# Kernel tuning notes

Measured on AMD Instinct MI355X. Metric: run time of the kernel, lower is better.

Reference implementation:

```python
import jax, jax.numpy as jnp
import numpy as np

D_MODEL = 1024
NUM_HEADS = 16


def setup_inputs() -> dict:
    key = jax.random.key(0)
    ks = jax.random.split(key, 5)
    B, S, D = 4, 2048, D_MODEL
    scale = 0.02  # realistic init scale so logits stay well-conditioned
    return {
        "x": jax.random.normal(ks[0], (B, S, D), dtype=jnp.float32),
        "Wq": jax.random.normal(ks[1], (D, D), dtype=jnp.float32) * scale,
        "Wk": jax.random.normal(ks[2], (D, D), dtype=jnp.float32) * scale,
        "Wv": jax.random.normal(ks[3], (D, D), dtype=jnp.float32) * scale,
        "Wo": jax.random.normal(ks[4], (D, D), dtype=jnp.float32) * scale,
    }


def reference(x, Wq, Wk, Wv, Wo):
    # x: (B, S, D). Weights are (d_out, d_in) as in the torch module.
    B, S, D = x.shape
    H = NUM_HEADS
    dk = D // H

    # Projections: einsum('oi,bli->blo') == x @ W.T
    q = jnp.einsum("oi,bsi->bso", Wq, x).reshape(B, S, H, dk).transpose(0, 2, 1, 3)
    k = jnp.einsum("oi,bsi->bso", Wk, x).reshape(B, S, H, dk).transpose(0, 2, 1, 3)
    v = jnp.einsum("oi,bsi->bso", Wv, x).reshape(B, S, H, dk).transpose(0, 2, 1, 3)

    # Scaled dot-product scores per head: (B, H, S, S)
    scores = jnp.einsum("bhqd,bhkd->bhqk", q, k) / jnp.sqrt(jnp.asarray(dk, x.dtype))

    # Causal mask (True = keep); masked entries get -inf (matches inf-subtraction)
    causal = jnp.tril(jnp.ones((S, S), dtype=bool))
    scores = jnp.where(causal, scores, -jnp.inf)

    attn = jax.nn.softmax(scores, axis=-1)

    out = jnp.einsum("bhqk,bhkd->bhqd", attn, v)  # (B, H, S, dk)
    out = out.transpose(0, 2, 1, 3).reshape(B, S, D)  # concat heads

    # Output projection: einsum('oi,bli->blo')
    return jnp.einsum("oi,bsi->bso", Wo, out)
```

## Files before the change

### kernel.cpp

```cpp
#include <hip/hip_runtime.h>
#include <hip/hip_bf16.h>

typedef unsigned short u16;
typedef __attribute__((ext_vector_type(8))) short short8;
typedef __attribute__((ext_vector_type(4))) float f32x4;

#if __has_builtin(__builtin_amdgcn_exp2f)
#define EXP2F(x) __builtin_amdgcn_exp2f(x)
#else
#define EXP2F(x) exp2f(x)
#endif

__device__ __forceinline__ float bf2f(u16 v) {
    union { unsigned u; float f; } c; c.u = ((unsigned)v) << 16; return c.f;
}
__device__ __forceinline__ u16 f2bf(float f) {
    union { float f; unsigned u; } c; c.f = f;
    unsigned r = c.u + 0x7fffu + ((c.u >> 16) & 1u);
    return (u16)(r >> 16);
}
__device__ __forceinline__ uint4 pack8(const float4 a, const float4 b) {
    uint4 r;
    r.x = (unsigned)f2bf(a.x) | ((unsigned)f2bf(a.y) << 16);
    r.y = (unsigned)f2bf(a.z) | ((unsigned)f2bf(a.w) << 16);
    r.z = (unsigned)f2bf(b.x) | ((unsigned)f2bf(b.y) << 16);
    r.w = (unsigned)f2bf(b.z) | ((unsigned)f2bf(b.w) << 16);
    return r;
}
__device__ __forceinline__ void gl_lds16(const u16* g, u16* l) {
    __builtin_amdgcn_global_load_lds((const __attribute__((address_space(1))) unsigned int*)g,
                                     (__attribute__((address_space(3))) unsigned int*)l, 16, 0, 0);
}

__global__ __launch_bounds__(256) void convert_all(const float* __restrict__ x,
                                                   const float* __restrict__ wq,
                                                   const float* __restrict__ wk,
                                                   const float* __restrict__ wv,
                                                   const float* __restrict__ wo,
                                                   u16* xb, u16* wqb, u16* wkb, u16* wvb, u16* wob) {
    size_t i8 = ((size_t)blockIdx.x * 256 + threadIdx.x) * 8;
    const float* src; u16* dst; size_t off;
    if (i8 < 8388608) { src = x; dst = xb; off = i8; }
    else {
        size_t idx = i8 - 8388608;
        int w = (int)(idx >> 20); off = idx & 1048575;
        src = (w == 0) ? wq : (w == 1) ? wk : (w == 2) ? wv : wo;
        dst = (w == 0) ? wqb : (w == 1) ? wkb : (w == 2) ? wvb : wob;
    }
    float4 a = *(const float4*)&src[off];
    float4 b = *(const float4*)&src[off + 4];
    *(uint4*)&dst[off] = pack8(a, b);
}

__device__ __forceinline__ void gemm_core(const u16* __restrict__ A, const u16* __restrict__ B,
                                          int m0, int n0, u16* As, u16* Bs, f32x4 acc[4][4]) {
    const int tid = threadIdx.x;
    const int wv = tid >> 6, lane = tid & 63, lr = lane & 15, quad = lane >> 4;
    const int srow = lane >> 3;
    const int scg  = (lane & 7) ^ srow;
    const int wm = (wv >> 1) * 64, wn = (wv & 1) * 64;

    for (int kt = 0; kt < 1024; kt += 64) {
        __syncthreads();
        #pragma unroll
        for (int t = 0; t < 4; ++t) {
            int r = wv * 32 + t * 8;
            gl_lds16(&A[(size_t)(m0 + r + srow) * 1024 + kt + scg * 8], &As[r * 64]);
            gl_lds16(&B[(size_t)(n0 + r + srow) * 1024 + kt + scg * 8], &Bs[r * 64]);
        }
        __syncthreads();
        #pragma unroll
        for (int c = 0; c < 2; ++c) {
            short8 af[4], bf[4];
            #pragma unroll
            for (int mi = 0; mi < 4; ++mi)
                af[mi] = *(const short8*)&As[(wm + mi * 16 + lr) * 64 + (((c * 4 + quad) ^ (lr & 7)) * 8)];
            #pragma unroll
            for (int ni = 0; ni < 4; ++ni)
                bf[ni] = *(const short8*)&Bs[(wn + ni * 16 + lr) * 64 + (((c * 4 + quad) ^ (lr & 7)) * 8)];
            #pragma unroll
            for (int mi = 0; mi < 4; ++mi)
                #pragma unroll
                for (int ni = 0; ni < 4; ++ni)
                    acc[mi][ni] = __builtin_amdgcn_mfma_f32_16x16x32_bf16(af[mi], bf[ni], acc[mi][ni], 0, 0, 0);
        }
    }
}

__device__ __forceinline__ void core_dual(const u16* __restrict__ A,
                                          const u16* __restrict__ B0,
                                          const u16* __restrict__ B1,
                                          int m0, int n0a, int n0b,
                                          u16* As, u16* Bs0, u16* Bs1,
                                          f32x4 acc0[2][4], f32x4 acc1[2][4]) {
    const int tid = threadIdx.x;
    const int wid = tid >> 6, lane = tid & 63, lr = lane & 15, quad = lane >> 4;
    const int srow = lane >> 3;
    const int scg  = (lane & 7) ^ srow;
    const int wm = (wid >> 1) * 32, wn = (wid & 1) * 64;
    const int r0 = wid * 16;

    for (int kt = 0; kt < 1024; kt += 64) {
        __syncthreads();
        #pragma unroll
        for (int h = 0; h < 2; ++h) {
            int r = r0 + h * 8;
            gl_lds16(&A [(size_t)(m0  + r + srow) * 1024 + kt + scg * 8], &As [r * 64]);
            gl_lds16(&B0[(size_t)(n0a + r + srow) * 1024 + kt + scg * 8], &Bs0[r * 64]);
            gl_lds16(&B1[(size_t)(n0b + r + srow) * 1024 + kt + scg * 8], &Bs1[r * 64]);
        }
        __syncthreads();
        #pragma unroll
        for (int c = 0; c < 2; ++c) {
            short8 af[2], bf[4];
            #pragma unroll
            for (int mi = 0; mi < 2; ++mi)
                af[mi] = *(const short8*)&As[(wm + mi * 16 + lr) * 64 + (((c * 4 + quad) ^ (lr & 7)) * 8)];
            #pragma unroll
            for (int ni = 0; ni < 4; ++ni)
                bf[ni] = *(const short8*)&Bs0[(wn + ni * 16 + lr) * 64 + (((c * 4 + quad) ^ (lr & 7)) * 8)];
            #pragma unroll
            for (int mi = 0; mi < 2; ++mi)
                #pragma unroll
                for (int ni = 0; ni < 4; ++ni)
                    acc0[mi][ni] = __builtin_amdgcn_mfma_f32_16x16x32_bf16(af[mi], bf[ni], acc0[mi][ni], 0, 0, 0);
            #pragma unroll
            for (int ni = 0; ni < 4; ++ni)
                bf[ni] = *(const short8*)&Bs1[(wn + ni * 16 + lr) * 64 + (((c * 4 + quad) ^ (lr & 7)) * 8)];
            #pragma unroll
            for (int mi = 0; mi < 2; ++mi)
                #pragma unroll
                for (int ni = 0; ni < 4; ++ni)
                    acc1[mi][ni] = __builtin_amdgcn_mfma_f32_16x16x32_bf16(af[mi], bf[ni], acc1[mi][ni], 0, 0, 0);
        }
    }
}

__global__ __launch_bounds__(512, 4) void gemm_qkv(const u16* __restrict__ xb,
                                                   const u16* __restrict__ wq,
                                                   const u16* __restrict__ wk,
                                                   const u16* __restrict__ wv,
                                                   u16* __restrict__ Qb, u16* __restrict__ Kb,
                                                   u16* __restrict__ Vtb) {
    __shared__ __align__(16) u16 As [8192];
    __shared__ __align__(16) u16 Bs0[8192];
    __shared__ __align__(16) u16 Bs1[8192];
    const int bid = blockIdx.x;

    f32x4 acc0[2][4], acc1[2][4];
    #pragma unroll
    for (int a = 0; a < 2; ++a)
        #pragma unroll
        for (int b = 0; b < 4; ++b) { acc0[a][b] = 0; acc1[a][b] = 0; }

    const int lane = threadIdx.x & 63, lr = lane & 15, quad = lane >> 4;
    const int wid = threadIdx.x >> 6;
    const int wm = (wid >> 1) * 32, wn = (wid & 1) * 64;

    if (bid < 512) {
        const int xcd = bid & 7;
        const int i   = bid >> 3;
        const int m0  = (xcd * 8 + (i & 7)) * 128;
        const int n0  = (i >> 3) * 128;
        core_dual(xb, wq, wk, m0, n0, n0, As, Bs0, Bs1, acc0, acc1);
        #pragma unroll
        for (int mi = 0; mi < 2; ++mi)
            #pragma unroll
            for (int ni = 0; ni < 4; ++ni)
                #pragma unroll
                for (int reg = 0; reg < 4; ++reg) {
                    int row = m0 + wm + mi * 16 + quad * 4 + reg;
                    int col = n0 + wn + ni * 16 + lr;
                    int bhh = (row >> 11) * 16 + (col >> 6);
                    size_t o = (size_t)bhh * 131072 + (size_t)(row & 2047) * 64 + (col & 63);
                    Qb[o] = f2bf(acc0[mi][ni][reg] * 0.18033688f);
                    Kb[o] = f2bf(acc1[mi][ni][reg]);
                }
    } else {
        const int t   = bid - 512;
        const int xcd = t & 7;
        const int j   = t >> 3;
        const int m0  = (j & 7) * 128;
        const int np  = xcd * 4 + (j >> 3);
        const int n0a = np * 256, n0b = np * 256 + 128;
        core_dual(wv, xb, xb, m0, n0a, n0b, As, Bs0, Bs1, acc0, acc1);
        #pragma unroll
        for (int half = 0; half < 2; ++half) {
            const int nb = half ? n0b : n0a;
            #pragma unroll
            for (int mi = 0; mi < 2; ++mi)
                #pragma unroll
                for (int ni = 0; ni < 4; ++ni)
                    #pragma unroll
                    for (int reg = 0; reg < 4; ++reg) {
                        int row = m0 + wm + mi * 16 + quad * 4 + reg;
                        int col = nb + wn + ni * 16 + lr;
                        int bhh = (col >> 11) * 16 + (row >> 6);
                        float v = half ? acc1[mi][ni][reg] : acc0[mi][ni][reg];
                        Vtb[(size_t)bhh * 131072 + (size_t)(row & 63) * 2048 + (col & 2047)] = f2bf(v);
                    }
        }
    }
}

__global__ __launch_bounds__(256) void gemm_out(const u16* __restrict__ Ob,
                                                const u16* __restrict__ wo,
                                                float* __restrict__ C) {
    __shared__ __align__(16) u16 As[8192];
    __shared__ __align__(16) u16 Bs[8192];
    const int bid = blockIdx.x;
    const int xcd = bid & 7;
    const int i   = bid >> 3;
    const int mp  = xcd * 8 + (i & 7);
    const int m0  = mp * 128, n0 = (i >> 3) * 128;

    f32x4 acc[4][4];
    #pragma unroll
    for (int a = 0; a < 4; ++a)
        #pragma unroll
        for (int j = 0; j < 4; ++j) acc[a][j] = 0;

    gemm_core(Ob, wo, m0, n0, As, Bs, acc);

    const int lane = threadIdx.x & 63, lr = lane & 15, quad = lane >> 4;
    const int wv4 = threadIdx.x >> 6;
    const int wm = (wv4 >> 1) * 64, wn = (wv4 & 1) * 64;
    #pragma unroll
    for (int mi = 0; mi < 4; ++mi)
        #pragma unroll
        for (int ni = 0; ni < 4; ++ni)
            #pragma unroll
            for (int reg = 0; reg < 4; ++reg) {
                int row = m0 + wm + mi * 16 + quad * 4 + reg;
                int col = n0 + wn + ni * 16 + lr;
                C[(size_t)row * 1024 + col] = acc[mi][ni][reg];
            }
}

__global__ __launch_bounds__(512, 4) void attn_flash(const u16* __restrict__ Q,
                                                     const u16* __restrict__ K,
                                                     const u16* __restrict__ Vt,
                                                     u16* __restrict__ O) {
    __shared__ __align__(16) u16 Kbuf[2][4096];
    __shared__ __align__(16) u16 Vbuf[2][4096];
    __shared__ __align__(16) u16 Ps[8][2048];

    const int tid = threadIdx.x, wave = tid >> 6, lane = tid & 63;
    const int lr = lane & 15, quad = lane >> 4;
    const int bh = blockIdx.x & 63;
    const int p  = blockIdx.x >> 6;
    const int qt8 = (p < 4) ? (7 - p) : (p - 4);
    const int qbase = qt8 * 256 + wave * 32;
    const size_t base = (size_t)bh * 131072;

    const int srow = lane >> 3;
    const int scg  = (lane & 7) ^ srow;

    const short8 onesv = {0x3f80, 0x3f80, 0x3f80, 0x3f80, 0x3f80, 0x3f80, 0x3f80, 0x3f80};

    short8 qf[2][2];
    #pragma unroll
    for (int qmi = 0; qmi < 2; ++qmi)
        #pragma unroll
        for (int c = 0; c < 2; ++c)
            qf[qmi][c] = *(const short8*)&Q[base + (size_t)(qbase + qmi * 16 + lr) * 64 + c * 32 + quad * 8];

    f32x4 oacc[4][2];
    #pragma unroll
    for (int i = 0; i < 4; ++i) { oacc[i][0] = 0; oacc[i][1] = 0; }
    f32x4 lacc[2];
    lacc[0] = 0; lacc[1] = 0;

    const int jmax = 4 * qt8 + 3;
    const int r0 = wave * 8;

    gl_lds16(&K[base + (size_t)(r0 + srow) * 64 + scg * 8], &Kbuf[0][r0 * 64]);
    gl_lds16(&Vt[base + (size_t)(r0 + srow) * 2048 + scg * 8], &Vbuf[0][r0 * 64]);

    for (int j = 0; j <= jmax; ++j) {
        const int buf = j & 1;
        __syncthreads();
        if (j < jmax) {
            const int nb = buf ^ 1;
            gl_lds16(&K[base + (size_t)((j + 1) * 64 + r0 + srow) * 64 + scg * 8], &Kbuf[nb][r0 * 64]);
            gl_lds16(&Vt[base + (size_t)(r0 + srow) * 2048 + (j + 1) * 64 + scg * 8], &Vbuf[nb][r0 * 64]);
        }

        if (j * 64 <= qbase + 31) {
            f32x4 st[4][2];
            #pragma unroll
            for (int ni = 0; ni < 4; ++ni) { st[ni][0] = 0; st[ni][1] = 0; }
            __builtin_amdgcn_s_setprio(1);
            #pragma unroll
            for (int c = 0; c < 2; ++c) {
                short8 kf[4];
                #pragma unroll
                for (int ni = 0; ni < 4; ++ni)
                    kf[ni] = *(const short8*)&Kbuf[buf][(ni * 16 + lr) * 64 + (((c * 4 + quad) ^ (lr & 7)) * 8)];
                #pragma unroll
                for (int ni = 0; ni < 4; ++ni)
                    #pragma unroll
                    for (int qmi = 0; qmi < 2; ++qmi)
                        st[ni][qmi] = __builtin_amdgcn_mfma_f32_16x16x32_bf16(kf[ni], qf[qmi][c], st[ni][qmi], 0, 0, 0);
            }
            __builtin_amdgcn_s_setprio(0);

            if (j >= 4 * qt8) {
                #pragma unroll
                for (int ni = 0; ni < 4; ++ni)
                    #pragma unroll
                    for (int qmi = 0; qmi < 2; ++qmi)
                        #pragma unroll
                        for (int reg = 0; reg < 4; ++reg) {
                            int key = j * 64 + ni * 16 + quad * 4 + reg;
                            int q   = qbase + qmi * 16 + lr;
                            if (key > q) st[ni][qmi][reg] = -3.0e38f;
                        }
            }

            #pragma unroll
            for (int qmi = 0; qmi < 2; ++qmi) {
                #pragma unroll
                for (int ni = 0; ni < 4; ++ni) {
                    unsigned u0 = __float_as_uint(EXP2F(st[ni][qmi][0]));
                    unsigned u1 = __float_as_uint(EXP2F(st[ni][qmi][1]));
                    unsigned u2 = __float_as_uint(EXP2F(st[ni][qmi][2]));
                    unsigned u3 = __float_as_uint(EXP2F(st[ni][qmi][3]));
                    uint2 pk;
                    pk.x = __builtin_amdgcn_perm(u1, u0, 0x07060302);
                    pk.y = __builtin_amdgcn_perm(u3, u2, 0x07060302);
                    int g8 = ni * 2 + (quad >> 1);
                    *(uint2*)&Ps[wave][qmi * 1024 + lr * 64 + ((g8 ^ (lr & 7)) * 8 + (quad & 1) * 4)] = pk;
                }
            }

            __builtin_amdgcn_s_setprio(1);
            #pragma unroll
            for (int c = 0; c < 2; ++c) {
                short8 pf[2];
                #pragma unroll
                for (int qmi = 0; qmi < 2; ++qmi)
                    pf[qmi] = *(const short8*)&Ps[wave][qmi * 1024 + lr * 64 + (((c * 4 + quad) ^ (lr & 7)) * 8)];
                #pragma unroll
                for (int dmi = 0; dmi < 4; ++dmi) {
                    short8 vf = *(const short8*)&Vbuf[buf][(dmi * 16 + lr) * 64 + (((c * 4 + quad) ^ (lr & 7)) * 8)];
                    #pragma unroll
                    for (int qmi = 0; qmi < 2; ++qmi)
                        oacc[dmi][qmi] = __builtin_amdgcn_mfma_f32_16x16x32_bf16(vf, pf[qmi], oacc[dmi][qmi], 0, 0, 0);
                }
                #pragma unroll
                for (int qmi = 0; qmi < 2; ++qmi)
                    lacc[qmi] = __builtin_amdgcn_mfma_f32_16x16x32_bf16(onesv, pf[qmi], lacc[qmi], 0, 0, 0);
            }
            __builtin_amdgcn_s_setprio(0);
        }
    }

    const int b = bh >> 4, h = bh & 15;
    #pragma unroll
    for (int qmi = 0; qmi < 2; ++qmi) {
        float rl = 1.0f / lacc[qmi][0];
        int s = qbase + qmi * 16 + lr;
        #pragma unroll
        for (int dmi = 0; dmi < 4; ++dmi) {
            unsigned o0 = f2bf(oacc[dmi][qmi][0] * rl);
            unsigned o1 = f2bf(oacc[dmi][qmi][1] * rl);
            unsigned o2 = f2bf(oacc[dmi][qmi][2] * rl);
            unsigned o3 = f2bf(oacc[dmi][qmi][3] * rl);
            uint2 pk;
            pk.x = o0 | (o1 << 16);
            pk.y = o2 | (o3 << 16);
            *(uint2*)&O[((size_t)(b * 2048 + s)) * 1024 + h * 64 + dmi * 16 + quad * 4] = pk;
        }
    }
}

extern "C" void kernel_launch(void* const* d_in, const int* in_sizes, int n_in,
                              void* d_out, int out_size, void* d_ws, size_t ws_size,
                              hipStream_t stream) {
    const float* x  = (const float*)d_in[0];
    const float* Wq = (const float*)d_in[1];
    const float* Wk = (const float*)d_in[2];
    const float* Wv = (const float*)d_in[3];
    const float* Wo = (const float*)d_in[4];

    u16* xb  = (u16*)d_ws;
    u16* wqb = xb + 8388608;
    u16* wkb = wqb + 1048576;
    u16* wvb = wkb + 1048576;
    u16* wob = wvb + 1048576;
    u16* Qb  = wob + 1048576;
    u16* Kb  = Qb + 8388608;
    u16* Vtb = Kb + 8388608;
    u16* Ob  = xb;

    convert_all<<<6144, 256, 0, stream>>>(x, Wq, Wk, Wv, Wo, xb, wqb, wkb, wvb, wob);

    gemm_qkv<<<768, 512, 0, stream>>>(xb, wqb, wkb, wvb, Qb, Kb, Vtb);

    attn_flash<<<512, 512, 0, stream>>>(Qb, Kb, Vtb, Ob);

    gemm_out<<<512, 256, 0, stream>>>(Ob, wob, (float*)d_out);
}
```

Measured before the change: 227.4 us.

## Fuse Q, K, V projections into one triple-accumulator GEMM sharing x tile

Replaces the split QKV kernel, where V was computed in separate blocks as Wv·xᵀ, with a single kernel where every block loads one x tile and three weight tiles and accumulates Q, K and V together. This removes redundant x loads and shrinks the grid from 768 to 512 uniform blocks. In exchange, shared memory and accumulator registers per block grow, and the transposed V store becomes strided and poorly coalesced.

```diff
diff --git a/kernel.cpp b/kernel.cpp
--- a/kernel.cpp
+++ b/kernel.cpp
@@ -87,12 +87,13 @@
     }
 }
 
-__device__ __forceinline__ void core_dual(const u16* __restrict__ A,
-                                          const u16* __restrict__ B0,
-                                          const u16* __restrict__ B1,
-                                          int m0, int n0a, int n0b,
-                                          u16* As, u16* Bs0, u16* Bs1,
-                                          f32x4 acc0[2][4], f32x4 acc1[2][4]) {
+__device__ __forceinline__ void core_triple(const u16* __restrict__ A,
+                                            const u16* __restrict__ B0,
+                                            const u16* __restrict__ B1,
+                                            const u16* __restrict__ B2,
+                                            int m0, int n0,
+                                            u16* As, u16* Bs0, u16* Bs1, u16* Bs2,
+                                            f32x4 acc0[2][4], f32x4 acc1[2][4], f32x4 acc2[2][4]) {
     const int tid = threadIdx.x;
     const int wid = tid >> 6, lane = tid & 63, lr = lane & 15, quad = lane >> 4;
     const int srow = lane >> 3;
@@ -105,9 +106,10 @@
         #pragma unroll
         for (int h = 0; h < 2; ++h) {
             int r = r0 + h * 8;
-            gl_lds16(&A [(size_t)(m0  + r + srow) * 1024 + kt + scg * 8], &As [r * 64]);
-            gl_lds16(&B0[(size_t)(n0a + r + srow) * 1024 + kt + scg * 8], &Bs0[r * 64]);
-            gl_lds16(&B1[(size_t)(n0b + r + srow) * 1024 + kt + scg * 8], &Bs1[r * 64]);
+            gl_lds16(&A [(size_t)(m0 + r + srow) * 1024 + kt + scg * 8], &As [r * 64]);
+            gl_lds16(&B0[(size_t)(n0 + r + srow) * 1024 + kt + scg * 8], &Bs0[r * 64]);
+            gl_lds16(&B1[(size_t)(n0 + r + srow) * 1024 + kt + scg * 8], &Bs1[r * 64]);
+            gl_lds16(&B2[(size_t)(n0 + r + srow) * 1024 + kt + scg * 8], &Bs2[r * 64]);
         }
         __syncthreads();
         #pragma unroll
@@ -132,6 +134,14 @@
                 #pragma unroll
                 for (int ni = 0; ni < 4; ++ni)
                     acc1[mi][ni] = __builtin_amdgcn_mfma_f32_16x16x32_bf16(af[mi], bf[ni], acc1[mi][ni], 0, 0, 0);
+            #pragma unroll
+            for (int ni = 0; ni < 4; ++ni)
+                bf[ni] = *(const short8*)&Bs2[(wn + ni * 16 + lr) * 64 + (((c * 4 + quad) ^ (lr & 7)) * 8)];
+            #pragma unroll
+            for (int mi = 0; mi < 2; ++mi)
+                #pragma unroll
+                for (int ni = 0; ni < 4; ++ni)
+                    acc2[mi][ni] = __builtin_amdgcn_mfma_f32_16x16x32_bf16(af[mi], bf[ni], acc2[mi][ni], 0, 0, 0);
         }
     }
 }
@@ -145,62 +155,39 @@
     __shared__ __align__(16) u16 As [8192];
     __shared__ __align__(16) u16 Bs0[8192];
     __shared__ __align__(16) u16 Bs1[8192];
+    __shared__ __align__(16) u16 Bs2[8192];
     const int bid = blockIdx.x;
-
-    f32x4 acc0[2][4], acc1[2][4];
+    const int xcd = bid & 7;
+    const int i   = bid >> 3;
+    const int m0  = (xcd * 8 + (i & 7)) * 128;
+    const int n0  = (i >> 3) * 128;
+
+    f32x4 acc0[2][4], acc1[2][4], acc2[2][4];
     #pragma unroll
     for (int a = 0; a < 2; ++a)
         #pragma unroll
-        for (int b = 0; b < 4; ++b) { acc0[a][b] = 0; acc1[a][b] = 0; }
+        for (int b = 0; b < 4; ++b) { acc0[a][b] = 0; acc1[a][b] = 0; acc2[a][b] = 0; }
+
+    core_triple(xb, wq, wk, wv, m0, n0, As, Bs0, Bs1, Bs2, acc0, acc1, acc2);
 
     const int lane = threadIdx.x & 63, lr = lane & 15, quad = lane >> 4;
     const int wid = threadIdx.x >> 6;
     const int wm = (wid >> 1) * 32, wn = (wid & 1) * 64;
-
-    if (bid < 512) {
-        const int xcd = bid & 7;
-        const int i   = bid >> 3;
-        const int m0  = (xcd * 8 + (i & 7)) * 128;
-        const int n0  = (i >> 3) * 128;
-        core_dual(xb, wq, wk, m0, n0, n0, As, Bs0, Bs1, acc0, acc1);
-        #pragma unroll
-        for (int mi = 0; mi < 2; ++mi)
-            #pragma unroll
-            for (int ni = 0; ni < 4; ++ni)
-                #pragma unroll
-                for (int reg = 0; reg < 4; ++reg) {
-                    int row = m0 + wm + mi * 16 + quad * 4 + reg;
-                    int col = n0 + wn + ni * 16 + lr;
-                    int bhh = (row >> 11) * 16 + (col >> 6);
-                    size_t o = (size_t)bhh * 131072 + (size_t)(row & 2047) * 64 + (col & 63);
-                    Qb[o] = f2bf(acc0[mi][ni][reg] * 0.18033688f);
-                    Kb[o] = f2bf(acc1[mi][ni][reg]);
-                }
-    } else {
-        const int t   = bid - 512;
-        const int xcd = t & 7;
-        const int j   = t >> 3;
-        const int m0  = (j & 7) * 128;
-        const int np  = xcd * 4 + (j >> 3);
-        const int n0a = np * 256, n0b = np * 256 + 128;
-        core_dual(wv, xb, xb, m0, n0a, n0b, As, Bs0, Bs1, acc0, acc1);
-        #pragma unroll
-        for (int half = 0; half < 2; ++half) {
-            const int nb = half ? n0b : n0a;
-            #pragma unroll
-            for (int mi = 0; mi < 2; ++mi)
-                #pragma unroll
-                for (int ni = 0; ni < 4; ++ni)
-                    #pragma unroll
-                    for (int reg = 0; reg < 4; ++reg) {
-                        int row = m0 + wm + mi * 16 + quad * 4 + reg;
-                        int col = nb + wn + ni * 16 + lr;
-                        int bhh = (col >> 11) * 16 + (row >> 6);
-                        float v = half ? acc1[mi][ni][reg] : acc0[mi][ni][reg];
-                        Vtb[(size_t)bhh * 131072 + (size_t)(row & 63) * 2048 + (col & 2047)] = f2bf(v);
-                    }
-        }
-    }
+    #pragma unroll
+    for (int mi = 0; mi < 2; ++mi)
+        #pragma unroll
+        for (int ni = 0; ni < 4; ++ni)
+            #pragma unroll
+            for (int reg = 0; reg < 4; ++reg) {
+                int row = m0 + wm + mi * 16 + quad * 4 + reg;
+                int col = n0 + wn + ni * 16 + lr;
+                int bhh = (row >> 11) * 16 + (col >> 6);
+                size_t o = (size_t)bhh * 131072 + (size_t)(row & 2047) * 64 + (col & 63);
+                Qb[o] = f2bf(acc0[mi][ni][reg] * 0.18033688f);
+                Kb[o] = f2bf(acc1[mi][ni][reg]);
+                Vtb[(size_t)bhh * 131072 + (size_t)(col & 63) * 2048 + (row & 2047)] =
+                    f2bf(acc2[mi][ni][reg]);
+            }
 }
 
 __global__ __launch_bounds__(256) void gemm_out(const u16* __restrict__ Ob,
@@ -396,7 +383,7 @@
 
     convert_all<<<6144, 256, 0, stream>>>(x, Wq, Wk, Wv, Wo, xb, wqb, wkb, wvb, wob);
 
-    gemm_qkv<<<768, 512, 0, stream>>>(xb, wqb, wkb, wvb, Qb, Kb, Vtb);
+    gemm_qkv<<<512, 512, 0, stream>>>(xb, wqb, wkb, wvb, Qb, Kb, Vtb);
 
     attn_flash<<<512, 512, 0, stream>>>(Qb, Kb, Vtb, Ob);
 
```

Result: slower. 254.2 us (+11.8%).
